# Kernel optimization log

Hardware: AMD Instinct MI355X
Metric: run time of the kernel (lower is better)

The kernel has to match this reference:

```python
import jax, jax.numpy as jnp
import numpy as np

D_MODEL = 1024
NUM_EXPERTS = 8


def setup_inputs() -> dict:
    key = jax.random.key(0)
    k_x, k_wg, k_bg, k_we, k_be = jax.random.split(key, 5)
    B, S, D, E = 4, 2048, D_MODEL, NUM_EXPERTS
    x = jax.random.normal(k_x, (B, S, D), dtype=jnp.float32)
    # gate: nn.Linear(d_model, num_experts) -> weight [E, D], bias [E]
    Wg = jax.random.normal(k_wg, (E, D), dtype=jnp.float32) * 0.02
    bg = jax.random.normal(k_bg, (E,), dtype=jnp.float32) * 0.02
    # experts: E x nn.Linear(d_model, d_model) -> weights [E, D, D], biases [E, D]
    We = jax.random.normal(k_we, (E, D, D), dtype=jnp.float32) * 0.02
    be = jax.random.normal(k_be, (E, D), dtype=jnp.float32) * 0.02
    return {"x": x, "Wg": Wg, "bg": bg, "We": We, "be": be, "top_k": 2}


def reference(x, Wg, bg, We, be, top_k):
    # gate_scores: softmax over experts. x:[B,S,D], Wg:[E,D] -> [B,S,E]
    gate_scores = jax.nn.softmax(jnp.einsum("bsd,ed->bse", x, Wg) + bg, axis=-1)
    top_k_values, top_k_indices = jax.lax.top_k(gate_scores, top_k)  # [B,S,K]
    # dense all-expert compute (faithful to original): [B,S,D,E]
    expert_outputs = jnp.einsum("bsd,ekd->bske", x, We) + be.T  # be.T: [D,E]
    # gather top-k experts along last dim: idx broadcast over feature dim D
    top_k_outputs = jnp.take_along_axis(
        expert_outputs, top_k_indices[:, :, None, :], axis=-1
    )  # [B,S,D,K]
    weighted = (top_k_outputs * top_k_values[:, :, None, :]).sum(axis=-1)  # [B,S,D]
    return weighted
```

## Files before the change

### kernel.cpp

```cpp
#include <hip/hip_runtime.h>
#include <hip/hip_bf16.h>
#include <stdint.h>

#define D_MODEL 1024
#define NUM_EXPERTS 8
#define NBUCKET 16
#define BM 128
#define BN 128
#define BK 64
#define KSTEPS (D_MODEL / BK)
#define GATE_TOK 32

typedef __bf16 bf16x8 __attribute__((ext_vector_type(8)));
typedef float f32x4 __attribute__((ext_vector_type(4)));
typedef unsigned short u16x8 __attribute__((ext_vector_type(8)));

__device__ __forceinline__ unsigned short f32_to_bf16_rne(float f) {
    union { float f; uint32_t u; } v;
    v.f = f;
    uint32_t u = v.u;
    u += 0x7FFFu + ((u >> 16) & 1u);
    return (unsigned short)(u >> 16);
}

__device__ __forceinline__ float bf16_to_f32(unsigned short h) {
    union { uint32_t u; float f; } v;
    v.u = ((uint32_t)h) << 16;
    return v.f;
}

__device__ __forceinline__ void gload_lds16(const unsigned short* g, unsigned short* l) {
    __builtin_amdgcn_global_load_lds(
        (const __attribute__((address_space(1))) void*)g,
        (__attribute__((address_space(3))) void*)l,
        16, 0, 0);
}

__global__ __launch_bounds__(256) void gate_kernel(
    const float* __restrict__ x, const float* __restrict__ Wg,
    const float* __restrict__ bg, int T,
    int* __restrict__ counts, int* __restrict__ token_list,
    float* __restrict__ gate_list, unsigned short* __restrict__ xb)
{
    const int tid  = threadIdx.x;
    const int lane = tid & 63;
    const int wave = tid >> 6;
    const int tokBase = blockIdx.x * GATE_TOK;

    __shared__ float4 WgS[NUM_EXPERTS * 256];
    __shared__ double logitS[GATE_TOK][NUM_EXPERTS];
    __shared__ int cntS[NBUCKET];
    __shared__ int baseS[NBUCKET];

    if (tid < NBUCKET) cntS[tid] = 0;
#pragma unroll
    for (int i = 0; i < 8; i++)
        WgS[i * 256 + tid] = ((const float4*)Wg)[i * 256 + tid];
    __syncthreads();

    for (int tt = 0; tt < GATE_TOK / 4; tt++) {
        const int lt = wave * (GATE_TOK / 4) + tt;
        const int token = tokBase + lt;
        const float4* xr4 = (const float4*)(x + (size_t)token * D_MODEL);
        ushort4* xbr4 = (ushort4*)(xb + (size_t)token * D_MODEL);

        float4 xv[4];
#pragma unroll
        for (int q = 0; q < 4; q++) {
            float4 f = xr4[q * 64 + lane];
            xv[q] = f;
            ushort4 o;
            o.x = f32_to_bf16_rne(f.x);
            o.y = f32_to_bf16_rne(f.y);
            o.z = f32_to_bf16_rne(f.z);
            o.w = f32_to_bf16_rne(f.w);
            xbr4[q * 64 + lane] = o;
        }

        double acc[NUM_EXPERTS];
#pragma unroll
        for (int e = 0; e < NUM_EXPERTS; e++) {
            double a = 0.0;
#pragma unroll
            for (int q = 0; q < 4; q++) {
                float4 w = WgS[e * 256 + q * 64 + lane];
                a += (double)xv[q].x * (double)w.x;
                a += (double)xv[q].y * (double)w.y;
                a += (double)xv[q].z * (double)w.z;
                a += (double)xv[q].w * (double)w.w;
            }
            acc[e] = a;
        }
#pragma unroll
        for (int e = 0; e < NUM_EXPERTS; e++) {
            double a = acc[e];
            for (int off = 32; off > 0; off >>= 1) a += __shfl_xor(a, off, 64);
            acc[e] = a;
        }
        if (lane == 0) {
#pragma unroll
            for (int e = 0; e < NUM_EXPERTS; e++)
                logitS[lt][e] = acc[e] + (double)bg[e];
        }
    }
    __syncthreads();

    int i1 = 0, i2 = 0, o1 = 0, o2 = 0;
    double v1d = 0.0, v2d = 0.0;
    const int token2 = tokBase + tid;
    if (tid < GATE_TOK) {
        double lg[NUM_EXPERTS];
#pragma unroll
        for (int e = 0; e < NUM_EXPERTS; e++) lg[e] = logitS[tid][e];
        i1 = 0;
#pragma unroll
        for (int e = 1; e < NUM_EXPERTS; e++) if (lg[e] > lg[i1]) i1 = e;
        i2 = (i1 == 0) ? 1 : 0;
#pragma unroll
        for (int e = 0; e < NUM_EXPERTS; e++)
            if (e != i1 && lg[e] > lg[i2]) i2 = e;
        double m = lg[i1], den = 0.0;
#pragma unroll
        for (int e = 0; e < NUM_EXPERTS; e++) den += exp(lg[e] - m);
        v1d = exp(lg[i1] - m) / den;
        v2d = exp(lg[i2] - m) / den;
        o1 = atomicAdd(&cntS[i1], 1);
        o2 = atomicAdd(&cntS[8 + i2], 1);
    }
    __syncthreads();
    if (tid < NBUCKET) baseS[tid] = atomicAdd(&counts[tid], cntS[tid]);
    __syncthreads();
    if (tid < GATE_TOK) {
        int p1 = i1 * T + baseS[i1] + o1;
        token_list[p1] = token2;
        gate_list[p1]  = (float)v1d;
        int p2 = (8 + i2) * T + baseS[8 + i2] + o2;
        token_list[p2] = token2;
        gate_list[p2]  = (float)v2d;
    }
}

__global__ __launch_bounds__(256) void convert_kernel(
    const float* __restrict__ src, unsigned short* __restrict__ dst)
{
    int gid = blockIdx.x * 256 + threadIdx.x;
    int s   = gid & 7;
    int n   = (gid >> 3) & 1023;
    int kt  = (gid >> 13) & (KSTEPS - 1);
    int e   = gid >> 17;

    const float* sp = src + ((size_t)(e * 1024 + n)) * 1024 + kt * BK + s * 8;
    float4 a = ((const float4*)sp)[0];
    float4 b = ((const float4*)sp)[1];
    u16x8 o;
    o[0] = f32_to_bf16_rne(a.x);
    o[1] = f32_to_bf16_rne(a.y);
    o[2] = f32_to_bf16_rne(a.z);
    o[3] = f32_to_bf16_rne(a.w);
    o[4] = f32_to_bf16_rne(b.x);
    o[5] = f32_to_bf16_rne(b.y);
    o[6] = f32_to_bf16_rne(b.z);
    o[7] = f32_to_bf16_rne(b.w);

    int ss = s ^ (n & 7);
    unsigned short* dp = dst + (((size_t)(e * KSTEPS + kt) * 1024 + n) * BK) + ss * 8;
    *(u16x8*)dp = o;
}

__global__ __launch_bounds__(256) void moe_gemm(
    const unsigned short* __restrict__ xb,
    const unsigned short* __restrict__ wb,
    const float* __restrict__ be,
    const int* __restrict__ counts,
    const int* __restrict__ token_list,
    const float* __restrict__ gate_list,
    unsigned short* __restrict__ ybuf,
    int T)
{
    const int bid = blockIdx.x;
    const int nt = bid & 7;
    const int rest = bid >> 3;
    const int vexp = rest & (NBUCKET - 1);
    const int mt = rest >> 4;
    const int e_w = vexp & 7;

    const int n_e = counts[vexp];
    const int m0 = mt * BM;
    if (m0 >= n_e) return;
    const int n0 = nt * BN;
    const int tid = threadIdx.x;

    __shared__ __align__(16) unsigned short As[2][BM * BK];
    __shared__ __align__(16) unsigned short Bs[2][BN * BK];
    __shared__ int   tokS[BM];
    __shared__ float gateS[BM];

    if (tid < BM) {
        int r = m0 + tid;
        int tk = 0; float gv = 0.f;
        if (r < n_e) {
            tk = token_list[vexp * T + r];
            gv = gate_list[vexp * T + r];
        }
        tokS[tid]  = tk;
        gateS[tid] = gv;
    }
    __syncthreads();

    const unsigned short* asrc[4];
#pragma unroll
    for (int i = 0; i < 4; i++) {
        int flat = i * 256 + tid;
        int r = flat >> 3, seg = flat & 7;
        int ss = seg ^ (r & 7);
        asrc[i] = xb + (size_t)tokS[r] * D_MODEL + ss * 8;
    }
    const unsigned short* bsrc =
        wb + (size_t)e_w * (KSTEPS * 1024 * BK) + (size_t)n0 * BK;

    const int wave = tid >> 6, lane = tid & 63;
    const int wm = (wave >> 1) * 64, wn = (wave & 1) * 64;
    const int frow = lane & 15;
    const int qq = lane >> 4;
    const int sw8 = frow & 7;

    f32x4 acc[4][4];
#pragma unroll
    for (int mi = 0; mi < 4; mi++)
#pragma unroll
        for (int ni = 0; ni < 4; ni++)
            acc[mi][ni] = (f32x4){0.f, 0.f, 0.f, 0.f};

#pragma unroll
    for (int i = 0; i < 4; i++) {
        int flat = i * 256 + tid;
        gload_lds16(asrc[i], &As[0][flat * 8]);
        gload_lds16(bsrc + flat * 8, &Bs[0][flat * 8]);
    }
    __syncthreads();

#pragma unroll 2
    for (int kt = 0; kt < KSTEPS; kt++) {
        const int cur = kt & 1;
        if (kt + 1 < KSTEPS) {
#pragma unroll
            for (int i = 0; i < 4; i++) {
                int flat = i * 256 + tid;
                gload_lds16(asrc[i] + (kt + 1) * BK, &As[cur ^ 1][flat * 8]);
                gload_lds16(bsrc + (size_t)(kt + 1) * (1024 * BK) + flat * 8,
                            &Bs[cur ^ 1][flat * 8]);
            }
        }
#pragma unroll
        for (int ks = 0; ks < 2; ks++) {
            const int off = ((ks * 4 + qq) ^ sw8) * 8;
            bf16x8 af[4], bfv[4];
#pragma unroll
            for (int mi = 0; mi < 4; mi++)
                af[mi] = *(const bf16x8*)&As[cur][(wm + mi * 16 + frow) * BK + off];
#pragma unroll
            for (int ni = 0; ni < 4; ni++)
                bfv[ni] = *(const bf16x8*)&Bs[cur][(wn + ni * 16 + frow) * BK + off];
#pragma unroll
            for (int mi = 0; mi < 4; mi++)
#pragma unroll
                for (int ni = 0; ni < 4; ni++)
                    acc[mi][ni] = __builtin_amdgcn_mfma_f32_16x16x32_bf16(
                        af[mi], bfv[ni], acc[mi][ni], 0, 0, 0);
        }
        __syncthreads();
    }

    unsigned short* ybase = ybuf + (size_t)(vexp >> 3) * T * D_MODEL;
    const int rbase = (lane >> 4) * 4;
    const int col   = lane & 15;
#pragma unroll
    for (int mi = 0; mi < 4; mi++) {
#pragma unroll
        for (int r = 0; r < 4; r++) {
            int lrow = wm + mi * 16 + rbase + r;
            if (m0 + lrow < n_e) {
                int   tk = tokS[lrow];
                float gv = gateS[lrow];
                unsigned short* yr = ybase + (size_t)tk * D_MODEL;
#pragma unroll
                for (int ni = 0; ni < 4; ni++) {
                    int c = n0 + wn + ni * 16 + col;
                    float val = gv * (acc[mi][ni][r] + be[e_w * D_MODEL + c]);
                    yr[c] = f32_to_bf16_rne(val);
                }
            }
        }
    }
}

__global__ __launch_bounds__(256) void combine_kernel(
    const unsigned short* __restrict__ y0,
    const unsigned short* __restrict__ y1,
    float* __restrict__ out, int n4)
{
    int i = blockIdx.x * 256 + threadIdx.x;
    if (i >= n4) return;
    ushort4 a = ((const ushort4*)y0)[i];
    ushort4 b = ((const ushort4*)y1)[i];
    float4 o;
    o.x = bf16_to_f32(a.x) + bf16_to_f32(b.x);
    o.y = bf16_to_f32(a.y) + bf16_to_f32(b.y);
    o.z = bf16_to_f32(a.z) + bf16_to_f32(b.z);
    o.w = bf16_to_f32(a.w) + bf16_to_f32(b.w);
    ((float4*)out)[i] = o;
}

extern "C" void kernel_launch(void* const* d_in, const int* in_sizes, int n_in,
                              void* d_out, int out_size, void* d_ws, size_t ws_size,
                              hipStream_t stream) {
    const float* x  = (const float*)d_in[0];
    const float* Wg = (const float*)d_in[1];
    const float* bg = (const float*)d_in[2];
    const float* We = (const float*)d_in[3];
    const float* be = (const float*)d_in[4];

    const int T = in_sizes[0] / D_MODEL;

    char* ws = (char*)d_ws;
    unsigned short* xb = (unsigned short*)ws;
    size_t off = (size_t)T * D_MODEL * 2;
    unsigned short* wbv = (unsigned short*)(ws + off);
    off += (size_t)NUM_EXPERTS * D_MODEL * D_MODEL * 2;
    int* counts = (int*)(ws + off);         off += 256;
    int* token_list = (int*)(ws + off);     off += (size_t)NBUCKET * T * 4;
    float* gate_list = (float*)(ws + off);  off += (size_t)NBUCKET * T * 4;
    unsigned short* ybuf = (unsigned short*)(ws + off);
    off += (size_t)2 * T * D_MODEL * 2;

    hipMemsetAsync(counts, 0, 256, stream);

    int nseg = NUM_EXPERTS * KSTEPS * 1024 * 8;
    convert_kernel<<<nseg / 256, 256, 0, stream>>>(We, wbv);

    gate_kernel<<<T / GATE_TOK, 256, 0, stream>>>(
        x, Wg, bg, T, counts, token_list, gate_list, xb);

    const int MT = (T + BM - 1) / BM;
    moe_gemm<<<MT * NBUCKET * 8, 256, 0, stream>>>(
        xb, wbv, be, counts, token_list, gate_list, ybuf, T);

    int n4c = T * D_MODEL / 4;
    combine_kernel<<<(n4c + 255) / 256, 256, 0, stream>>>(
        ybuf, ybuf + (size_t)T * D_MODEL, (float*)d_out, n4c);
}
```

Before: 214.6 us.

## Fuse weight conversion into gate kernel and make GEMM and combine grid-stride

The separate fp32-to-bf16 weight conversion kernel is merged into the gating kernel as extra blocks, so routing and conversion run in one launch and can overlap. The conversion now reads the weights contiguously and scatters the swizzled writes. The gate tile shrinks to 16 tokens per block. The MoE GEMM becomes a fixed-grid, grid-stride loop over work tiles, so most empty tiles are never launched as blocks. The combine kernel also uses a fixed grid. The hardcoded gate block count assumes T=8192, and the persistent loop adds per-tile barriers.

```diff
diff --git a/kernel.cpp b/kernel.cpp
--- a/kernel.cpp
+++ b/kernel.cpp
@@ -9,7 +9,11 @@
 #define BN 128
 #define BK 64
 #define KSTEPS (D_MODEL / BK)
-#define GATE_TOK 32
+#define GATE_TOK 16
+#define GATE_BLOCKS 512
+#define CONV_BLOCKS 4096
+#define GEMM_GRID 2048
+#define NWORK 8192
 
 typedef __bf16 bf16x8 __attribute__((ext_vector_type(8)));
 typedef float f32x4 __attribute__((ext_vector_type(4)));
@@ -36,13 +40,42 @@
         16, 0, 0);
 }
 
-__global__ __launch_bounds__(256) void gate_kernel(
+__global__ __launch_bounds__(256) void prep_kernel(
     const float* __restrict__ x, const float* __restrict__ Wg,
-    const float* __restrict__ bg, int T,
+    const float* __restrict__ bg, const float* __restrict__ We, int T,
     int* __restrict__ counts, int* __restrict__ token_list,
-    float* __restrict__ gate_list, unsigned short* __restrict__ xb)
+    float* __restrict__ gate_list, unsigned short* __restrict__ xb,
+    unsigned short* __restrict__ wbv)
 {
-    const int tid  = threadIdx.x;
+    const int tid = threadIdx.x;
+
+    if (blockIdx.x >= GATE_BLOCKS) {
+        int g = (blockIdx.x - GATE_BLOCKS) * 256 + tid;
+        int s   = g & 7;
+        int kt  = (g >> 3) & (KSTEPS - 1);
+        int n   = (g >> 7) & 1023;
+        int e   = g >> 17;
+
+        const float* sp = We + (size_t)g * 8;
+        float4 a = ((const float4*)sp)[0];
+        float4 b = ((const float4*)sp)[1];
+        u16x8 o;
+        o[0] = f32_to_bf16_rne(a.x);
+        o[1] = f32_to_bf16_rne(a.y);
+        o[2] = f32_to_bf16_rne(a.z);
+        o[3] = f32_to_bf16_rne(a.w);
+        o[4] = f32_to_bf16_rne(b.x);
+        o[5] = f32_to_bf16_rne(b.y);
+        o[6] = f32_to_bf16_rne(b.z);
+        o[7] = f32_to_bf16_rne(b.w);
+
+        int ss = s ^ (n & 7);
+        unsigned short* dp =
+            wbv + (((size_t)(e * KSTEPS + kt) * 1024 + n) * BK) + ss * 8;
+        *(u16x8*)dp = o;
+        return;
+    }
+
     const int lane = tid & 63;
     const int wave = tid >> 6;
     const int tokBase = blockIdx.x * GATE_TOK;
@@ -140,33 +173,6 @@
     }
 }
 
-__global__ __launch_bounds__(256) void convert_kernel(
-    const float* __restrict__ src, unsigned short* __restrict__ dst)
-{
-    int gid = blockIdx.x * 256 + threadIdx.x;
-    int s   = gid & 7;
-    int n   = (gid >> 3) & 1023;
-    int kt  = (gid >> 13) & (KSTEPS - 1);
-    int e   = gid >> 17;
-
-    const float* sp = src + ((size_t)(e * 1024 + n)) * 1024 + kt * BK + s * 8;
-    float4 a = ((const float4*)sp)[0];
-    float4 b = ((const float4*)sp)[1];
-    u16x8 o;
-    o[0] = f32_to_bf16_rne(a.x);
-    o[1] = f32_to_bf16_rne(a.y);
-    o[2] = f32_to_bf16_rne(a.z);
-    o[3] = f32_to_bf16_rne(a.w);
-    o[4] = f32_to_bf16_rne(b.x);
-    o[5] = f32_to_bf16_rne(b.y);
-    o[6] = f32_to_bf16_rne(b.z);
-    o[7] = f32_to_bf16_rne(b.w);
-
-    int ss = s ^ (n & 7);
-    unsigned short* dp = dst + (((size_t)(e * KSTEPS + kt) * 1024 + n) * BK) + ss * 8;
-    *(u16x8*)dp = o;
-}
-
 __global__ __launch_bounds__(256) void moe_gemm(
     const unsigned short* __restrict__ xb,
     const unsigned short* __restrict__ wb,
@@ -177,117 +183,120 @@
     unsigned short* __restrict__ ybuf,
     int T)
 {
-    const int bid = blockIdx.x;
-    const int nt = bid & 7;
-    const int rest = bid >> 3;
-    const int vexp = rest & (NBUCKET - 1);
-    const int mt = rest >> 4;
-    const int e_w = vexp & 7;
-
-    const int n_e = counts[vexp];
-    const int m0 = mt * BM;
-    if (m0 >= n_e) return;
-    const int n0 = nt * BN;
     const int tid = threadIdx.x;
-
-    __shared__ __align__(16) unsigned short As[2][BM * BK];
-    __shared__ __align__(16) unsigned short Bs[2][BN * BK];
-    __shared__ int   tokS[BM];
-    __shared__ float gateS[BM];
-
-    if (tid < BM) {
-        int r = m0 + tid;
-        int tk = 0; float gv = 0.f;
-        if (r < n_e) {
-            tk = token_list[vexp * T + r];
-            gv = gate_list[vexp * T + r];
-        }
-        tokS[tid]  = tk;
-        gateS[tid] = gv;
-    }
-    __syncthreads();
-
-    const unsigned short* asrc[4];
-#pragma unroll
-    for (int i = 0; i < 4; i++) {
-        int flat = i * 256 + tid;
-        int r = flat >> 3, seg = flat & 7;
-        int ss = seg ^ (r & 7);
-        asrc[i] = xb + (size_t)tokS[r] * D_MODEL + ss * 8;
-    }
-    const unsigned short* bsrc =
-        wb + (size_t)e_w * (KSTEPS * 1024 * BK) + (size_t)n0 * BK;
-
     const int wave = tid >> 6, lane = tid & 63;
     const int wm = (wave >> 1) * 64, wn = (wave & 1) * 64;
     const int frow = lane & 15;
     const int qq = lane >> 4;
     const int sw8 = frow & 7;
 
-    f32x4 acc[4][4];
-#pragma unroll
-    for (int mi = 0; mi < 4; mi++)
-#pragma unroll
-        for (int ni = 0; ni < 4; ni++)
-            acc[mi][ni] = (f32x4){0.f, 0.f, 0.f, 0.f};
-
-#pragma unroll
-    for (int i = 0; i < 4; i++) {
-        int flat = i * 256 + tid;
-        gload_lds16(asrc[i], &As[0][flat * 8]);
-        gload_lds16(bsrc + flat * 8, &Bs[0][flat * 8]);
-    }
-    __syncthreads();
+    __shared__ __align__(16) unsigned short As[2][BM * BK];
+    __shared__ __align__(16) unsigned short Bs[2][BN * BK];
+    __shared__ int   tokS[BM];
+    __shared__ float gateS[BM];
+
+    for (int work = blockIdx.x; work < NWORK; work += GEMM_GRID) {
+        const int nt = work & 7;
+        const int rest = work >> 3;
+        const int vexp = rest & (NBUCKET - 1);
+        const int mt = rest >> 4;
+        const int e_w = vexp & 7;
+
+        const int n_e = counts[vexp];
+        const int m0 = mt * BM;
+        if (m0 >= n_e) continue;
+        const int n0 = nt * BN;
+
+        __syncthreads();
+
+        if (tid < BM) {
+            int r = m0 + tid;
+            int tk = 0; float gv = 0.f;
+            if (r < n_e) {
+                tk = token_list[vexp * T + r];
+                gv = gate_list[vexp * T + r];
+            }
+            tokS[tid]  = tk;
+            gateS[tid] = gv;
+        }
+        __syncthreads();
+
+        const unsigned short* asrc[4];
+#pragma unroll
+        for (int i = 0; i < 4; i++) {
+            int flat = i * 256 + tid;
+            int r = flat >> 3, seg = flat & 7;
+            int ss = seg ^ (r & 7);
+            asrc[i] = xb + (size_t)tokS[r] * D_MODEL + ss * 8;
+        }
+        const unsigned short* bsrc =
+            wb + (size_t)e_w * (KSTEPS * 1024 * BK) + (size_t)n0 * BK;
+
+        f32x4 acc[4][4];
+#pragma unroll
+        for (int mi = 0; mi < 4; mi++)
+#pragma unroll
+            for (int ni = 0; ni < 4; ni++)
+                acc[mi][ni] = (f32x4){0.f, 0.f, 0.f, 0.f};
+
+#pragma unroll
+        for (int i = 0; i < 4; i++) {
+            int flat = i * 256 + tid;
+            gload_lds16(asrc[i], &As[0][flat * 8]);
+            gload_lds16(bsrc + flat * 8, &Bs[0][flat * 8]);
+        }
+        __syncthreads();
 
 #pragma unroll 2
-    for (int kt = 0; kt < KSTEPS; kt++) {
-        const int cur = kt & 1;
-        if (kt + 1 < KSTEPS) {
-#pragma unroll
-            for (int i = 0; i < 4; i++) {
-                int flat = i * 256 + tid;
-                gload_lds16(asrc[i] + (kt + 1) * BK, &As[cur ^ 1][flat * 8]);
-                gload_lds16(bsrc + (size_t)(kt + 1) * (1024 * BK) + flat * 8,
-                            &Bs[cur ^ 1][flat * 8]);
-            }
-        }
-#pragma unroll
-        for (int ks = 0; ks < 2; ks++) {
-            const int off = ((ks * 4 + qq) ^ sw8) * 8;
-            bf16x8 af[4], bfv[4];
-#pragma unroll
-            for (int mi = 0; mi < 4; mi++)
-                af[mi] = *(const bf16x8*)&As[cur][(wm + mi * 16 + frow) * BK + off];
-#pragma unroll
-            for (int ni = 0; ni < 4; ni++)
-                bfv[ni] = *(const bf16x8*)&Bs[cur][(wn + ni * 16 + frow) * BK + off];
-#pragma unroll
-            for (int mi = 0; mi < 4; mi++)
+        for (int kt = 0; kt < KSTEPS; kt++) {
+            const int cur = kt & 1;
+            if (kt + 1 < KSTEPS) {
+#pragma unroll
+                for (int i = 0; i < 4; i++) {
+                    int flat = i * 256 + tid;
+                    gload_lds16(asrc[i] + (kt + 1) * BK, &As[cur ^ 1][flat * 8]);
+                    gload_lds16(bsrc + (size_t)(kt + 1) * (1024 * BK) + flat * 8,
+                                &Bs[cur ^ 1][flat * 8]);
+                }
+            }
+#pragma unroll
+            for (int ks = 0; ks < 2; ks++) {
+                const int off = ((ks * 4 + qq) ^ sw8) * 8;
+                bf16x8 af[4], bfv[4];
+#pragma unroll
+                for (int mi = 0; mi < 4; mi++)
+                    af[mi] = *(const bf16x8*)&As[cur][(wm + mi * 16 + frow) * BK + off];
 #pragma unroll
                 for (int ni = 0; ni < 4; ni++)
-                    acc[mi][ni] = __builtin_amdgcn_mfma_f32_16x16x32_bf16(
-                        af[mi], bfv[ni], acc[mi][ni], 0, 0, 0);
-        }
-        __syncthreads();
-    }
-
-    unsigned short* ybase = ybuf + (size_t)(vexp >> 3) * T * D_MODEL;
-    const int rbase = (lane >> 4) * 4;
-    const int col   = lane & 15;
-#pragma unroll
-    for (int mi = 0; mi < 4; mi++) {
-#pragma unroll
-        for (int r = 0; r < 4; r++) {
-            int lrow = wm + mi * 16 + rbase + r;
-            if (m0 + lrow < n_e) {
-                int   tk = tokS[lrow];
-                float gv = gateS[lrow];
-                unsigned short* yr = ybase + (size_t)tk * D_MODEL;
-#pragma unroll
-                for (int ni = 0; ni < 4; ni++) {
-                    int c = n0 + wn + ni * 16 + col;
-                    float val = gv * (acc[mi][ni][r] + be[e_w * D_MODEL + c]);
-                    yr[c] = f32_to_bf16_rne(val);
+                    bfv[ni] = *(const bf16x8*)&Bs[cur][(wn + ni * 16 + frow) * BK + off];
+#pragma unroll
+                for (int mi = 0; mi < 4; mi++)
+#pragma unroll
+                    for (int ni = 0; ni < 4; ni++)
+                        acc[mi][ni] = __builtin_amdgcn_mfma_f32_16x16x32_bf16(
+                            af[mi], bfv[ni], acc[mi][ni], 0, 0, 0);
+            }
+            __syncthreads();
+        }
+
+        unsigned short* ybase = ybuf + (size_t)(vexp >> 3) * T * D_MODEL;
+        const int rbase = (lane >> 4) * 4;
+        const int col   = lane & 15;
+#pragma unroll
+        for (int mi = 0; mi < 4; mi++) {
+#pragma unroll
+            for (int r = 0; r < 4; r++) {
+                int lrow = wm + mi * 16 + rbase + r;
+                if (m0 + lrow < n_e) {
+                    int   tk = tokS[lrow];
+                    float gv = gateS[lrow];
+                    unsigned short* yr = ybase + (size_t)tk * D_MODEL;
+#pragma unroll
+                    for (int ni = 0; ni < 4; ni++) {
+                        int c = n0 + wn + ni * 16 + col;
+                        float val = gv * (acc[mi][ni][r] + be[e_w * D_MODEL + c]);
+                        yr[c] = f32_to_bf16_rne(val);
+                    }
                 }
             }
         }
@@ -299,16 +308,16 @@
     const unsigned short* __restrict__ y1,
     float* __restrict__ out, int n4)
 {
-    int i = blockIdx.x * 256 + threadIdx.x;
-    if (i >= n4) return;
-    ushort4 a = ((const ushort4*)y0)[i];
-    ushort4 b = ((const ushort4*)y1)[i];
-    float4 o;
-    o.x = bf16_to_f32(a.x) + bf16_to_f32(b.x);
-    o.y = bf16_to_f32(a.y) + bf16_to_f32(b.y);
-    o.z = bf16_to_f32(a.z) + bf16_to_f32(b.z);
-    o.w = bf16_to_f32(a.w) + bf16_to_f32(b.w);
-    ((float4*)out)[i] = o;
+    for (int i = blockIdx.x * 256 + threadIdx.x; i < n4; i += 2048 * 256) {
+        ushort4 a = ((const ushort4*)y0)[i];
+        ushort4 b = ((const ushort4*)y1)[i];
+        float4 o;
+        o.x = bf16_to_f32(a.x) + bf16_to_f32(b.x);
+        o.y = bf16_to_f32(a.y) + bf16_to_f32(b.y);
+        o.z = bf16_to_f32(a.z) + bf16_to_f32(b.z);
+        o.w = bf16_to_f32(a.w) + bf16_to_f32(b.w);
+        ((float4*)out)[i] = o;
+    }
 }
 
 extern "C" void kernel_launch(void* const* d_in, const int* in_sizes, int n_in,
@@ -335,17 +344,13 @@
 
     hipMemsetAsync(counts, 0, 256, stream);
 
-    int nseg = NUM_EXPERTS * KSTEPS * 1024 * 8;
-    convert_kernel<<<nseg / 256, 256, 0, stream>>>(We, wbv);
-
-    gate_kernel<<<T / GATE_TOK, 256, 0, stream>>>(
-        x, Wg, bg, T, counts, token_list, gate_list, xb);
-
-    const int MT = (T + BM - 1) / BM;
-    moe_gemm<<<MT * NBUCKET * 8, 256, 0, stream>>>(
+    prep_kernel<<<GATE_BLOCKS + CONV_BLOCKS, 256, 0, stream>>>(
+        x, Wg, bg, We, T, counts, token_list, gate_list, xb, wbv);
+
+    moe_gemm<<<GEMM_GRID, 256, 0, stream>>>(
         xb, wbv, be, counts, token_list, gate_list, ybuf, T);
 
     int n4c = T * D_MODEL / 4;
-    combine_kernel<<<(n4c + 255) / 256, 256, 0, stream>>>(
+    combine_kernel<<<2048, 256, 0, stream>>>(
         ybuf, ybuf + (size_t)T * D_MODEL, (float*)d_out, n4c);
 }
```

New measurement: 222.2 us. 3.5% more time.

## Fuse expert weight bf16 conversion into MoE GEMM and widen gate blocks

Applied to the files above, without the earlier changes.

Drops the separate convert_kernel that pre-converted all expert weights to a swizzled bf16 buffer. The GEMM now loads fp32 weights into registers, converts them after the MFMA phase, and writes them swizzled into LDS, with sched_barriers keeping the loads ahead of the math. This removes a full pass over the weights and its workspace, but every GEMM tile now reads fp32 weights, twice the bytes, repeatedly across M tiles. It also adds conversion ALU work and register pressure, and replaces the direct-to-LDS weight loads. The gate kernel is also changed to 512 threads per block, so each wave handles fewer tokens.

```diff
diff --git a/kernel.cpp b/kernel.cpp
--- a/kernel.cpp
+++ b/kernel.cpp
@@ -36,7 +36,7 @@
         16, 0, 0);
 }
 
-__global__ __launch_bounds__(256) void gate_kernel(
+__global__ __launch_bounds__(512) void gate_kernel(
     const float* __restrict__ x, const float* __restrict__ Wg,
     const float* __restrict__ bg, int T,
     int* __restrict__ counts, int* __restrict__ token_list,
@@ -54,12 +54,12 @@
 
     if (tid < NBUCKET) cntS[tid] = 0;
 #pragma unroll
-    for (int i = 0; i < 8; i++)
-        WgS[i * 256 + tid] = ((const float4*)Wg)[i * 256 + tid];
-    __syncthreads();
-
-    for (int tt = 0; tt < GATE_TOK / 4; tt++) {
-        const int lt = wave * (GATE_TOK / 4) + tt;
+    for (int i = 0; i < 4; i++)
+        WgS[i * 512 + tid] = ((const float4*)Wg)[i * 512 + tid];
+    __syncthreads();
+
+    for (int tt = 0; tt < GATE_TOK / 8; tt++) {
+        const int lt = wave * (GATE_TOK / 8) + tt;
         const int token = tokBase + lt;
         const float4* xr4 = (const float4*)(x + (size_t)token * D_MODEL);
         ushort4* xbr4 = (ushort4*)(xb + (size_t)token * D_MODEL);
@@ -140,36 +140,9 @@
     }
 }
 
-__global__ __launch_bounds__(256) void convert_kernel(
-    const float* __restrict__ src, unsigned short* __restrict__ dst)
-{
-    int gid = blockIdx.x * 256 + threadIdx.x;
-    int s   = gid & 7;
-    int n   = (gid >> 3) & 1023;
-    int kt  = (gid >> 13) & (KSTEPS - 1);
-    int e   = gid >> 17;
-
-    const float* sp = src + ((size_t)(e * 1024 + n)) * 1024 + kt * BK + s * 8;
-    float4 a = ((const float4*)sp)[0];
-    float4 b = ((const float4*)sp)[1];
-    u16x8 o;
-    o[0] = f32_to_bf16_rne(a.x);
-    o[1] = f32_to_bf16_rne(a.y);
-    o[2] = f32_to_bf16_rne(a.z);
-    o[3] = f32_to_bf16_rne(a.w);
-    o[4] = f32_to_bf16_rne(b.x);
-    o[5] = f32_to_bf16_rne(b.y);
-    o[6] = f32_to_bf16_rne(b.z);
-    o[7] = f32_to_bf16_rne(b.w);
-
-    int ss = s ^ (n & 7);
-    unsigned short* dp = dst + (((size_t)(e * KSTEPS + kt) * 1024 + n) * BK) + ss * 8;
-    *(u16x8*)dp = o;
-}
-
 __global__ __launch_bounds__(256) void moe_gemm(
     const unsigned short* __restrict__ xb,
-    const unsigned short* __restrict__ wb,
+    const float* __restrict__ We,
     const float* __restrict__ be,
     const int* __restrict__ counts,
     const int* __restrict__ token_list,
@@ -208,15 +181,18 @@
     __syncthreads();
 
     const unsigned short* asrc[4];
+    const float* wsrc[4];
+    int bdst[4];
 #pragma unroll
     for (int i = 0; i < 4; i++) {
         int flat = i * 256 + tid;
         int r = flat >> 3, seg = flat & 7;
         int ss = seg ^ (r & 7);
         asrc[i] = xb + (size_t)tokS[r] * D_MODEL + ss * 8;
-    }
-    const unsigned short* bsrc =
-        wb + (size_t)e_w * (KSTEPS * 1024 * BK) + (size_t)n0 * BK;
+        wsrc[i] = We + (size_t)e_w * (D_MODEL * D_MODEL)
+                     + (size_t)(n0 + r) * D_MODEL + seg * 8;
+        bdst[i] = r * BK + ss * 8;
+    }
 
     const int wave = tid >> 6, lane = tid & 63;
     const int wm = (wave >> 1) * 64, wn = (wave & 1) * 64;
@@ -231,11 +207,26 @@
         for (int ni = 0; ni < 4; ni++)
             acc[mi][ni] = (f32x4){0.f, 0.f, 0.f, 0.f};
 
+    float4 p0[4], p1[4];
 #pragma unroll
     for (int i = 0; i < 4; i++) {
+        p0[i] = ((const float4*)wsrc[i])[0];
+        p1[i] = ((const float4*)wsrc[i])[1];
         int flat = i * 256 + tid;
         gload_lds16(asrc[i], &As[0][flat * 8]);
-        gload_lds16(bsrc + flat * 8, &Bs[0][flat * 8]);
+    }
+#pragma unroll
+    for (int i = 0; i < 4; i++) {
+        u16x8 h;
+        h[0] = f32_to_bf16_rne(p0[i].x);
+        h[1] = f32_to_bf16_rne(p0[i].y);
+        h[2] = f32_to_bf16_rne(p0[i].z);
+        h[3] = f32_to_bf16_rne(p0[i].w);
+        h[4] = f32_to_bf16_rne(p1[i].x);
+        h[5] = f32_to_bf16_rne(p1[i].y);
+        h[6] = f32_to_bf16_rne(p1[i].z);
+        h[7] = f32_to_bf16_rne(p1[i].w);
+        *(u16x8*)&Bs[0][bdst[i]] = h;
     }
     __syncthreads();
 
@@ -245,12 +236,15 @@
         if (kt + 1 < KSTEPS) {
 #pragma unroll
             for (int i = 0; i < 4; i++) {
+                const float* wp = wsrc[i] + (kt + 1) * BK;
+                p0[i] = ((const float4*)wp)[0];
+                p1[i] = ((const float4*)wp)[1];
                 int flat = i * 256 + tid;
                 gload_lds16(asrc[i] + (kt + 1) * BK, &As[cur ^ 1][flat * 8]);
-                gload_lds16(bsrc + (size_t)(kt + 1) * (1024 * BK) + flat * 8,
-                            &Bs[cur ^ 1][flat * 8]);
             }
         }
+        __builtin_amdgcn_sched_barrier(0);
+
 #pragma unroll
         for (int ks = 0; ks < 2; ks++) {
             const int off = ((ks * 4 + qq) ^ sw8) * 8;
@@ -267,6 +261,23 @@
                 for (int ni = 0; ni < 4; ni++)
                     acc[mi][ni] = __builtin_amdgcn_mfma_f32_16x16x32_bf16(
                         af[mi], bfv[ni], acc[mi][ni], 0, 0, 0);
+        }
+        __builtin_amdgcn_sched_barrier(0);
+
+        if (kt + 1 < KSTEPS) {
+#pragma unroll
+            for (int i = 0; i < 4; i++) {
+                u16x8 h;
+                h[0] = f32_to_bf16_rne(p0[i].x);
+                h[1] = f32_to_bf16_rne(p0[i].y);
+                h[2] = f32_to_bf16_rne(p0[i].z);
+                h[3] = f32_to_bf16_rne(p0[i].w);
+                h[4] = f32_to_bf16_rne(p1[i].x);
+                h[5] = f32_to_bf16_rne(p1[i].y);
+                h[6] = f32_to_bf16_rne(p1[i].z);
+                h[7] = f32_to_bf16_rne(p1[i].w);
+                *(u16x8*)&Bs[cur ^ 1][bdst[i]] = h;
+            }
         }
         __syncthreads();
     }
@@ -325,8 +336,6 @@
     char* ws = (char*)d_ws;
     unsigned short* xb = (unsigned short*)ws;
     size_t off = (size_t)T * D_MODEL * 2;
-    unsigned short* wbv = (unsigned short*)(ws + off);
-    off += (size_t)NUM_EXPERTS * D_MODEL * D_MODEL * 2;
     int* counts = (int*)(ws + off);         off += 256;
     int* token_list = (int*)(ws + off);     off += (size_t)NBUCKET * T * 4;
     float* gate_list = (float*)(ws + off);  off += (size_t)NBUCKET * T * 4;
@@ -335,15 +344,12 @@
 
     hipMemsetAsync(counts, 0, 256, stream);
 
-    int nseg = NUM_EXPERTS * KSTEPS * 1024 * 8;
-    convert_kernel<<<nseg / 256, 256, 0, stream>>>(We, wbv);
-
-    gate_kernel<<<T / GATE_TOK, 256, 0, stream>>>(
+    gate_kernel<<<T / GATE_TOK, 512, 0, stream>>>(
         x, Wg, bg, T, counts, token_list, gate_list, xb);
 
     const int MT = (T + BM - 1) / BM;
     moe_gemm<<<MT * NBUCKET * 8, 256, 0, stream>>>(
-        xb, wbv, be, counts, token_list, gate_list, ybuf, T);
+        xb, We, be, counts, token_list, gate_list, ybuf, T);
 
     int n4c = T * D_MODEL / 4;
     combine_kernel<<<(n4c + 255) / 256, 256, 0, stream>>>(
```

Result: slower. 263.7 us (+22.9%).
